# Kernel tuning notes

Measured on AMD Instinct MI355X. Metric: run time of the kernel, lower is better.

The kernel has to match this reference:

```python
import jax, jax.numpy as jnp
import numpy as np

K = 11          # target_size = len(tag_to_idx)
START = 10      # tag_to_idx['START']
STOP = 9        # tag_to_idx['STOP']
NEG = -10000.0
B, T = 4096, 2048


def setup_inputs() -> dict:
    key = jax.random.key(0)
    k1, k2, k3 = jax.random.split(key, 3)
    feats = jax.random.normal(k1, (B, T, K), dtype=jnp.float32)
    # body tags only (START/STOP never appear in gold sequences)
    tags = jax.random.randint(k2, (B, T), 0, 9)
    transitions = jax.random.uniform(k3, (K, K), dtype=jnp.float32)
    # constraints set in __init__: nothing transitions into START; STOP emits nothing
    transitions = transitions.at[START, :].set(NEG).at[:, STOP].set(NEG)
    return {"feats": feats, "tags": tags, "transitions": transitions}


def _nll_one(feats, tags, trans):
    # feats: [T, K], tags: [T] -> scalar negative log-likelihood
    init = jnp.full((K,), NEG, dtype=feats.dtype).at[START].set(0.0)

    def step(fv, feat):
        # tag_var[next, prev] = fv[prev] + trans[next, prev] + feat[next]
        tag_var = fv[None, :] + trans + feat[:, None]
        return jax.nn.logsumexp(tag_var, axis=1), None

    fv, _ = jax.lax.scan(step, init, feats)
    forward_score = jax.nn.logsumexp(fv + trans[STOP])

    start_tags = jnp.concatenate([jnp.array([START], dtype=tags.dtype), tags])
    stop_tags = jnp.concatenate([tags, jnp.array([STOP], dtype=tags.dtype)])
    gold = trans[stop_tags, start_tags].sum() + feats[jnp.arange(feats.shape[0]), tags].sum()
    return forward_score - gold


def reference(feats, tags, transitions):
    # per-sentence CRF NLL (forward_score - gold_score), vmapped over the batch
    return jax.vmap(lambda f, t: _nll_one(f, t, transitions))(feats, tags)
```

## Files before the change

kernel.cpp:

```cpp
#include <hip/hip_runtime.h>

#define K 11
#define TT 2048
#define NB (TT / 16)
#define START_TAG 10
#define STOP_TAG 9
#define L2E 1.4426950408889634f
#define LN2 0.6931471805599453f

template<int S>
__device__ __forceinline__ float ror16(float x) {
    return __int_as_float(__builtin_amdgcn_update_dpp(
        __float_as_int(x), __float_as_int(x), 0x120 + S, 0xF, 0xF, false));
}

__global__ __launch_bounds__(256, 1) void crf_nll_kernel(
    const float* __restrict__ feats,
    const int* __restrict__ tags,
    const float* __restrict__ trans,
    float* __restrict__ out,
    int nseq)
{
    __shared__ float T2[K * 16];
    if (threadIdx.x < K * 16) {
        int r = threadIdx.x >> 4, c = threadIdx.x & 15;
        T2[threadIdx.x] = (c < K) ? trans[r * K + c] : 0.0f;
    }
    __syncthreads();

    const int tid = blockIdx.x * blockDim.x + threadIdx.x;
    const int n = threadIdx.x & 15;
    const int seq = tid >> 4;
    if (seq >= nseq) return;
    const int st = (n < K) ? n : n - K;

    float w[16];
#pragma unroll
    for (int s = 0; s < 16; ++s) w[s] = 0.0f;
#pragma unroll
    for (int r = 0; r < K; ++r) {
        int p = st + r; if (p >= K) p -= K;
        float e = __builtin_amdgcn_exp2f(trans[st * K + p] * L2E);
        int s = (r == 0) ? 0 : ((n + r <= 15) ? r : r + 5);
        w[s] = e;
    }
    const float pstop =
        (n < K) ? __builtin_amdgcn_exp2f(trans[STOP_TAG * K + st] * L2E) : 0.0f;

    const float* fb = feats + (size_t)seq * TT * K;
    const int* tb = tags + (size_t)seq * TT;

    float a = (n == START_TAG) ? 1.0f : 0.0f;
    int cacc = 0;
    float goldt = 0.0f, goldf = 0.0f;
    int prev = START_TAG;

    float fA[16], fB[16];
    int gA[16], gB[16];

    auto prefetch = [&](float (&f)[16], int (&g)[16], int blk) {
        const float* fp = fb + (size_t)blk * 16 * K + st;
#pragma unroll
        for (int j = 0; j < 16; ++j) f[j] = fp[j * K];
        const int4* tp = (const int4*)(tb + blk * 16);
#pragma unroll
        for (int q = 0; q < 4; ++q) {
            int4 u = tp[q];
            g[4 * q + 0] = u.x; g[4 * q + 1] = u.y;
            g[4 * q + 2] = u.z; g[4 * q + 3] = u.w;
        }
    };

    auto process = [&](float (&f)[16], int (&g)[16]) {
        float tv[16];
        {
            int pv = prev;
#pragma unroll
            for (int j = 0; j < 16; ++j) {
                tv[j] = T2[(g[j] << 4) + pv];
                pv = g[j];
            }
        }
        float e[16];
#pragma unroll
        for (int j = 0; j < 16; ++j)
            e[j] = __builtin_amdgcn_exp2f(f[j] * L2E);
#pragma unroll
        for (int j = 0; j < 16; ++j) {
            float av = a;
            float acc0 = w[0] * av;
            float acc1 = w[1] * ror16<1>(av);
            float acc2 = w[2] * ror16<2>(av);
            float acc3 = w[3] * ror16<3>(av);
            acc0 = fmaf(w[4],  ror16<4>(av),  acc0);
            acc1 = fmaf(w[5],  ror16<5>(av),  acc1);
            acc2 = fmaf(w[6],  ror16<6>(av),  acc2);
            acc3 = fmaf(w[7],  ror16<7>(av),  acc3);
            acc0 = fmaf(w[8],  ror16<8>(av),  acc0);
            acc1 = fmaf(w[9],  ror16<9>(av),  acc1);
            acc2 = fmaf(w[10], ror16<10>(av), acc2);
            acc3 = fmaf(w[11], ror16<11>(av), acc3);
            acc0 = fmaf(w[12], ror16<12>(av), acc0);
            acc1 = fmaf(w[13], ror16<13>(av), acc1);
            acc2 = fmaf(w[14], ror16<14>(av), acc2);
            acc3 = fmaf(w[15], ror16<15>(av), acc3);
            float S = (acc0 + acc1) + (acc2 + acc3);
            a = S * e[j];
            if ((j & 7) == 7) {
                float m = a;
                m = fmaxf(m, ror16<1>(m));
                m = fmaxf(m, ror16<2>(m));
                m = fmaxf(m, ror16<4>(m));
                m = fmaxf(m, ror16<8>(m));
                int ex = ((__float_as_int(m) >> 23) & 0xFF) - 127;
                a *= __int_as_float((127 - ex) << 23);
                cacc += ex;
            }
        }
        float gt = 0.0f, gf = 0.0f;
#pragma unroll
        for (int j = 0; j < 16; ++j) {
            gt += tv[j];
            gf += (n == g[j]) ? f[j] : 0.0f;
        }
        goldt += gt;
        goldf += gf;
        prev = g[15];
    };

    prefetch(fA, gA, 0);
#pragma unroll 1
    for (int b = 0; b < NB; b += 2) {
        int b1 = (b + 1 < NB) ? b + 1 : NB - 1;
        prefetch(fB, gB, b1);
        process(fA, gA);
        int b2 = (b + 2 < NB) ? b + 2 : NB - 1;
        prefetch(fA, gA, b2);
        process(fB, gB);
    }

    float wv = a * pstop;
    wv += ror16<1>(wv);
    wv += ror16<2>(wv);
    wv += ror16<4>(wv);
    wv += ror16<8>(wv);
    float fs = (__builtin_amdgcn_logf(wv) + (float)cacc) * LN2;

    goldf += ror16<1>(goldf);
    goldf += ror16<2>(goldf);
    goldf += ror16<4>(goldf);
    goldf += ror16<8>(goldf);

    float gold = goldt + goldf + T2[STOP_TAG * 16 + prev];
    if (n == 0) out[seq] = fs - gold;
}

extern "C" void kernel_launch(void* const* d_in, const int* in_sizes, int n_in,
                              void* d_out, int out_size, void* d_ws, size_t ws_size,
                              hipStream_t stream) {
    const float* feats = (const float*)d_in[0];
    const int* tags = (const int*)d_in[1];
    const float* trans = (const float*)d_in[2];
    float* out = (float*)d_out;
    const int nseq = in_sizes[1] / TT;
    const int threads = 256;
    const int blocks = (nseq * 16 + threads - 1) / threads;
    hipLaunchKernelGGL(crf_nll_kernel, dim3(blocks), dim3(threads), 0, stream,
                       feats, tags, trans, out, nseq);
}
```

Baseline: 672.2 us.

## Split each CRF sequence into forward and backward halves meeting in the middle

After: 630.6 us. 1.07x faster.

```diff
diff --git a/kernel.cpp b/kernel.cpp
--- a/kernel.cpp
+++ b/kernel.cpp
@@ -2,7 +2,7 @@
 
 #define K 11
 #define TT 2048
-#define NB (TT / 16)
+#define NBH 64
 #define START_TAG 10
 #define STOP_TAG 9
 #define L2E 1.4426950408889634f
@@ -14,23 +14,26 @@
         __float_as_int(x), __float_as_int(x), 0x120 + S, 0xF, 0xF, false));
 }
 
-__global__ __launch_bounds__(256, 1) void crf_nll_kernel(
+__global__ __launch_bounds__(256, 2) void crf_nll_kernel(
     const float* __restrict__ feats,
     const int* __restrict__ tags,
     const float* __restrict__ trans,
     float* __restrict__ out,
     int nseq)
 {
-    __shared__ float T2[K * 16];
+    __shared__ float Tf[K * 16];
+    __shared__ float Tb[K * 16];
     if (threadIdx.x < K * 16) {
         int r = threadIdx.x >> 4, c = threadIdx.x & 15;
-        T2[threadIdx.x] = (c < K) ? trans[r * K + c] : 0.0f;
+        Tf[threadIdx.x] = (c < K) ? trans[r * K + c] : 0.0f;
+        Tb[threadIdx.x] = (c < K) ? trans[c * K + r] : 0.0f;
     }
     __syncthreads();
 
     const int tid = blockIdx.x * blockDim.x + threadIdx.x;
     const int n = threadIdx.x & 15;
-    const int seq = tid >> 4;
+    const int bwd = (tid >> 4) & 1;
+    const int seq = tid >> 5;
     if (seq >= nseq) return;
     const int st = (n < K) ? n : n - K;
 
@@ -40,35 +43,53 @@
 #pragma unroll
     for (int r = 0; r < K; ++r) {
         int p = st + r; if (p >= K) p -= K;
-        float e = __builtin_amdgcn_exp2f(trans[st * K + p] * L2E);
+        float tw = bwd ? trans[p * K + st] : trans[st * K + p];
+        float e = __builtin_amdgcn_exp2f(tw * L2E);
         int s = (r == 0) ? 0 : ((n + r <= 15) ? r : r + 5);
         w[s] = e;
     }
-    const float pstop =
-        (n < K) ? __builtin_amdgcn_exp2f(trans[STOP_TAG * K + st] * L2E) : 0.0f;
 
     const float* fb = feats + (size_t)seq * TT * K;
     const int* tb = tags + (size_t)seq * TT;
+    const float* Tg = bwd ? Tb : Tf;
 
-    float a = (n == START_TAG) ? 1.0f : 0.0f;
+    const float fl = fb[(size_t)(TT - 1) * K + st];
+    const int gl = tb[TT - 1];
+
+    float a;
+    int prev;
+    float goldt, goldf;
+    if (bwd) {
+        a = __builtin_amdgcn_exp2f((trans[STOP_TAG * K + st] + fl) * L2E);
+        prev = gl;
+        goldt = Tf[STOP_TAG * 16 + gl];
+        goldf = (n == gl) ? fl : 0.0f;
+    } else {
+        a = (n == START_TAG) ? 1.0f : 0.0f;
+        prev = START_TAG;
+        goldt = 0.0f;
+        goldf = 0.0f;
+    }
     int cacc = 0;
-    float goldt = 0.0f, goldf = 0.0f;
-    int prev = START_TAG;
 
     float fA[16], fB[16];
     int gA[16], gB[16];
 
     auto prefetch = [&](float (&f)[16], int (&g)[16], int blk) {
-        const float* fp = fb + (size_t)blk * 16 * K + st;
+        const int base_row = bwd ? (2031 - (blk << 4)) : (blk << 4);
+        const float* fp = fb + (size_t)base_row * K + st;
+        const int* tp = tb + base_row;
+        float tf[16]; int tg[16];
 #pragma unroll
-        for (int j = 0; j < 16; ++j) f[j] = fp[j * K];
-        const int4* tp = (const int4*)(tb + blk * 16);
+        for (int j = 0; j < 16; ++j) tf[j] = fp[j * K];
 #pragma unroll
-        for (int q = 0; q < 4; ++q) {
-            int4 u = tp[q];
-            g[4 * q + 0] = u.x; g[4 * q + 1] = u.y;
-            g[4 * q + 2] = u.z; g[4 * q + 3] = u.w;
+        for (int j = 0; j < 16; ++j) tg[j] = tp[j];
+#pragma unroll
+        for (int j = 0; j < 16; ++j) {
+            f[j] = bwd ? tf[15 - j] : tf[j];
+            g[j] = bwd ? tg[15 - j] : tg[j];
         }
+        if (blk == NBH - 1 && bwd) f[15] = 0.0f;
     };
 
     auto process = [&](float (&f)[16], int (&g)[16]) {
@@ -77,7 +98,7 @@
             int pv = prev;
 #pragma unroll
             for (int j = 0; j < 16; ++j) {
-                tv[j] = T2[(g[j] << 4) + pv];
+                tv[j] = Tg[(g[j] << 4) + pv];
                 pv = g[j];
             }
         }
@@ -130,29 +151,33 @@
 
     prefetch(fA, gA, 0);
 #pragma unroll 1
-    for (int b = 0; b < NB; b += 2) {
-        int b1 = (b + 1 < NB) ? b + 1 : NB - 1;
+    for (int b = 0; b < NBH; b += 2) {
+        int b1 = (b + 1 < NBH) ? b + 1 : NBH - 1;
         prefetch(fB, gB, b1);
         process(fA, gA);
-        int b2 = (b + 2 < NB) ? b + 2 : NB - 1;
+        int b2 = (b + 2 < NBH) ? b + 2 : NBH - 1;
         prefetch(fA, gA, b2);
         process(fB, gB);
     }
 
-    float wv = a * pstop;
-    wv += ror16<1>(wv);
-    wv += ror16<2>(wv);
-    wv += ror16<4>(wv);
-    wv += ror16<8>(wv);
-    float fs = (__builtin_amdgcn_logf(wv) + (float)cacc) * LN2;
+    float v = (n < K) ? a : 0.0f;
+    float pv2 = __shfl_xor(v, 16);
+    float prod = v * pv2;
+    prod += ror16<1>(prod);
+    prod += ror16<2>(prod);
+    prod += ror16<4>(prod);
+    prod += ror16<8>(prod);
+    int ctot = cacc + __shfl_xor(cacc, 16);
+    float fs = (__builtin_amdgcn_logf(prod) + (float)ctot) * LN2;
 
     goldf += ror16<1>(goldf);
     goldf += ror16<2>(goldf);
     goldf += ror16<4>(goldf);
     goldf += ror16<8>(goldf);
+    float G = goldt + goldf;
+    G += __shfl_xor(G, 16);
 
-    float gold = goldt + goldf + T2[STOP_TAG * 16 + prev];
-    if (n == 0) out[seq] = fs - gold;
+    if ((threadIdx.x & 31) == 0) out[seq] = fs - G;
 }
 
 extern "C" void kernel_launch(void* const* d_in, const int* in_sizes, int n_in,
@@ -164,7 +189,7 @@
     float* out = (float*)d_out;
     const int nseq = in_sizes[1] / TT;
     const int threads = 256;
-    const int blocks = (nseq * 16 + threads - 1) / threads;
+    const int blocks = (nseq * 32 + threads - 1) / threads;
     hipLaunchKernelGGL(crf_nll_kernel, dim3(blocks), dim3(threads), 0, stream,
                        feats, tags, trans, out, nseq);
 }
```
